# Performance work log

Hardware: AMD Instinct MI355X
Metric: run time of the kernel (lower is better)

The kernel has to match this reference:

```python
import jax, jax.numpy as jnp
import numpy as np
from jax import lax

B, T, N, NIN, NOUT = 16, 32, 512, 32, 16
STEEP_GJ, STEEP_FIRE, STEEP_IN = 10.0, 10.0, 5.0
INPUT_THRESH, LEAKY_SLOPE = 0.01, 0.01
EDGE_P = 0.05


def setup_inputs() -> dict:
    key = jax.random.key(0)
    ks = jax.random.split(key, 7)
    obs_sequence = jax.random.normal(ks[0], (B, T, NIN), dtype=jnp.float32)
    weights = jax.random.uniform(ks[1], (N, N), dtype=jnp.float32) * 5.0
    thresholds = jax.random.uniform(ks[2], (N,), dtype=jnp.float32) * 5.0
    decay = jax.random.uniform(ks[3], (N,), dtype=jnp.float32) * 0.5
    mask_ex = jax.random.bernoulli(ks[4], EDGE_P, (N, N)).astype(jnp.float32)
    mask_in = jax.random.bernoulli(ks[5], EDGE_P, (N, N)).astype(jnp.float32)
    mask_gj = jax.random.bernoulli(ks[6], EDGE_P, (N, N)).astype(jnp.float32)
    input_indices = jnp.arange(NIN, dtype=jnp.int32)
    output_indices = NIN + jnp.arange(NOUT, dtype=jnp.int32)
    return {"obs_sequence": obs_sequence, "weights": weights, "thresholds": thresholds,
            "decay": decay, "mask_ex": mask_ex, "mask_in": mask_in, "mask_gj": mask_gj,
            "input_indices": input_indices, "output_indices": output_indices}


def reference(obs_sequence, weights, thresholds, decay, mask_ex, mask_in, mask_gj,
              input_indices, output_indices):
    # obs_encoder and action_decoder are identity: obs values drive input neurons,
    # action = E-state of output neurons.
    W_pos = jax.nn.softplus(weights)            # [N,N] (dst, src)
    W_chem = W_pos * (mask_ex - mask_in)        # excitatory minus inhibitory
    W_gj = W_pos * mask_gj                      # gap junctions

    def step(carry, obs_t):
        E, O = carry                            # [B,N] each
        O_h = O.at[:, input_indices].set(obs_t)
        E_h = E.at[:, input_indices].set(obs_t)
        # chemical synapse current: [B,N] @ [N,N]^T
        I_chem = O_h @ W_chem.T
        # gap junction current via O(B,N,N) broadcast, as in original
        diff = O_h[:, None, :] - E_h[:, :, None]          # [B, dst, src]
        direction = jnp.tanh(STEEP_GJ * diff)
        I_gj = jnp.einsum('ds,bs,bds->bd', W_gj, O_h, direction)
        curr = jnp.clip(E_h + I_chem + I_gj, -10.0, 10.0)
        z = curr - thresholds
        O_new = jnp.where(z >= 0, z, LEAKY_SLOPE * z)      # leaky_relu
        firing_gate = jax.nn.sigmoid(STEEP_FIRE * z)
        decay_gate = jax.nn.sigmoid(STEEP_IN * (jnp.abs(E_h - curr) - INPUT_THRESH))
        E_nonfired = decay_gate * curr + (1.0 - decay_gate) * (E_h - decay)
        E_new = firing_gate * O_new + (1.0 - firing_gate) * E_nonfired
        O_new = O_new.at[:, input_indices].set(obs_t)
        E_new = E_new.at[:, input_indices].set(obs_t)
        action = E_new[:, output_indices]
        return (E_new, O_new), action

    b, n = obs_sequence.shape[0], weights.shape[0]
    E0 = jnp.zeros((b, n), dtype=obs_sequence.dtype)
    O0 = jnp.zeros((b, n), dtype=obs_sequence.dtype)
    (_, _), actions = lax.scan(step, (E0, O0), jnp.swapaxes(obs_sequence, 0, 1))
    return jnp.swapaxes(actions, 0, 1)                    # [B,T,NOUT]
```

## Files before the change

kernel.cpp:

```cpp
#include <hip/hip_runtime.h>

#define N_NEUR 512
#define B_SZ   16
#define T_STEPS 32
#define NIN    32
#define NOUT   16
#define CAPC   84
#define CAPG   52
#define MC     42
#define MG     26
#define MCP    21
#define MGP    13
#define SLACKC 6
#define SLACKG 6
#define LOG2E  1.4426950408889634f

__device__ __forceinline__ float rcp_fast(float x) {
#if __has_builtin(__builtin_amdgcn_rcpf)
    return __builtin_amdgcn_rcpf(x);
#else
    return 1.0f / x;
#endif
}
__device__ __forceinline__ float exp2_fast(float x) {
#if __has_builtin(__builtin_amdgcn_exp2f)
    return __builtin_amdgcn_exp2f(x);
#else
    return exp2f(x);
#endif
}
__device__ __forceinline__ float pair_swap(float x) {
#if __has_builtin(__builtin_amdgcn_mov_dpp)
    return __int_as_float(__builtin_amdgcn_mov_dpp(__float_as_int(x), 0xB1, 0xF, 0xF, true));
#else
    return __shfl_xor(x, 1);
#endif
}

__global__ __launch_bounds__(64) void prep1_kernel(
    const float* __restrict__ W,
    const float* __restrict__ mex,
    const float* __restrict__ min_,
    const float* __restrict__ mgj,
    int* __restrict__ key_arr, int* __restrict__ ccA, int* __restrict__ cgA,
    int2* __restrict__ tmpC, int2* __restrict__ tmpG)
{
    const int row  = blockIdx.x;
    const int lane = threadIdx.x;
    const unsigned long long below = (1ull << lane) - 1ull;
    int bc = 0, bg = 0;
    for (int c0 = 0; c0 < N_NEUR; c0 += 64) {
        const int col = c0 + lane;
        const int off = row * N_NEUR + col;
        const float w  = W[off];
        const float sp = fmaxf(w, 0.0f) + log1pf(__expf(-fabsf(w)));
        const float dm = mex[off] - min_[off];
        bool a = (dm != 0.0f);
        unsigned long long m = __ballot(a);
        int idx = bc + __popcll(m & below);
        if (a && idx < CAPC)
            tmpC[row * CAPC + idx] = make_int2(col, __float_as_int(sp * dm));
        bc += __popcll(m);

        const float g = mgj[off];
        bool ag = (g != 0.0f);
        m = __ballot(ag);
        idx = bg + __popcll(m & below);
        if (ag && idx < CAPG)
            tmpG[row * CAPG + idx] = make_int2(col, __float_as_int(sp * g));
        bg += __popcll(m);
    }
    if (lane == 0) {
        int cc = min(bc, CAPC), cg = min(bg, CAPG);
        ccA[row] = cc; cgA[row] = cg; key_arr[row] = cc + cg;
    }
}

__global__ __launch_bounds__(512) void rank_kernel(
    int* __restrict__ key_then_rank,
    const int* __restrict__ ccA, const int* __restrict__ cgA,
    int* __restrict__ order, int* __restrict__ mCwA, int* __restrict__ mGwA)
{
    __shared__ int keyS[N_NEUR];
    __shared__ int mxc[16], mxg[16];
    const int d = threadIdx.x;
    keyS[d] = key_then_rank[d];
    if (d < 16) { mxc[d] = 0; mxg[d] = 0; }
    __syncthreads();
    const int kd = keyS[d];
    int r = 0;
    #pragma unroll 8
    for (int j = 0; j < N_NEUR; ++j) {
        int kj = keyS[j];
        r += (kj < kd) || (kj == kd && j < d);
    }
    order[r] = d;
    key_then_rank[d] = r;
    atomicMax(&mxc[r >> 5], ccA[d]);
    atomicMax(&mxg[r >> 5], cgA[d]);
    __syncthreads();
    if (d < 16) {
        int mc = ((mxc[d] + 1) >> 1) + SLACKC;
        mc = (mc + 3) & ~3;
        mCwA[d] = min(mc, MC);
        int mg = ((mxg[d] + 1) >> 1) + SLACKG;
        mg = (mg + 3) & ~3;
        mGwA[d] = min(mg, MG);
    }
}

__global__ __launch_bounds__(64) void prep2_kernel(
    const int* __restrict__ rankA, const int* __restrict__ ccA, const int* __restrict__ cgA,
    const int* __restrict__ mCwA, const int* __restrict__ mGwA,
    const int2* __restrict__ tmpC, const int2* __restrict__ tmpG,
    float* __restrict__ wCt, unsigned* __restrict__ cpCt,
    float* __restrict__ wGt, unsigned* __restrict__ cpGt)
{
    __shared__ int   cS[CAPC];  __shared__ float wS[CAPC];
    __shared__ int   cSg[CAPG]; __shared__ float wSg[CAPG];
    __shared__ int   keyS[MC];
    __shared__ int   scol[MC];  __shared__ float sw[MC];
    __shared__ float wOut[MC];  __shared__ int   oOut[MC];
    const int d    = blockIdx.x;
    const int lane = threadIdx.x;
    const int r    = rankA[d];
    const int wv   = r >> 5;
    const int Lb   = 2 * (r & 31);
    const int cc = ccA[d], cg = cgA[d];
    const int Mc = mCwA[wv], Mg = mGwA[wv];

    for (int k = lane; k < CAPC; k += 64) {
        int2 e = (k < cc) ? tmpC[d * CAPC + k] : make_int2(0, 0);
        cS[k] = e.x; wS[k] = __int_as_float(e.y);
    }
    for (int k = lane; k < CAPG; k += 64) {
        int2 e = (k < cg) ? tmpG[d * CAPG + k] : make_int2(0, 0);
        cSg[k] = e.x; wSg[k] = __int_as_float(e.y);
    }
    __syncthreads();

    #pragma unroll
    for (int task = 0; task < 4; ++task) {
        const int isG  = task >> 1, h = task & 1;
        const int cnt  = isG ? cg : cc;
        const int m    = (cnt + 1 - h) >> 1;
        const int M    = isG ? Mg : Mc;
        const int Mcap = isG ? MG : MC;
        const int MPc  = isG ? MGP : MCP;
        const int myL  = Lb + h;

        int col = 0; float w = 0.0f; int key = 0;
        if (lane < m) {
            col = isG ? cSg[2 * lane + h] : cS[2 * lane + h];
            w   = isG ? wSg[2 * lane + h] : wS[2 * lane + h];
            key = ((col & 31) - myL) & 31;
            keyS[lane] = key;
        }
        __syncthreads();
        if (lane < m) {
            int rk = 0;
            for (int j = 0; j < m; ++j) {
                int kj = keyS[j];
                rk += (kj < key) || (kj == key && j < lane);
            }
            scol[rk] = col; sw[rk] = w;
        }
        if (lane < Mcap) {
            wOut[lane] = 0.0f;
            int bk = (((lane * 32) / M) + myL) & 31;
            oOut[lane] = bk << 2;
        }
        __syncthreads();

        int a = -(1 << 28);
        int colj = 0; float wj = 0.0f;
        if (lane < m) {
            colj = scol[lane]; wj = sw[lane];
            int kj = ((colj & 31) - myL) & 31;
            a = ((kj * M) >> 5) - lane;
        }
        #pragma unroll
        for (int o = 1; o < 64; o <<= 1) {
            int t2 = __shfl_up(a, o);
            if (lane >= o) a = max(a, t2);
        }
        if (lane < m) {
            int slot = min(lane + a, M - m + lane);
            wOut[slot] = wj;
            oOut[slot] = colj << 2;
        }
        __syncthreads();

        float*    wT = isG ? wGt  : wCt;
        unsigned* cT = isG ? cpGt : cpCt;
        if (lane < Mcap)
            wT[(wv * Mcap + lane) * 64 + myL] = wOut[lane];
        if (lane < MPc) {
            unsigned c0 = (unsigned)oOut[2 * lane];
            unsigned c1 = (unsigned)oOut[2 * lane + 1];
            cT[(wv * MPc + lane) * 64 + myL] = c0 | (c1 << 16);
        }
        __syncthreads();
    }
}

#define CHEM_K(k, A) {                                                      \
    unsigned pk = cpC[(k) >> 1];                                            \
    unsigned off = ((k) & 1) ? (pk >> 16) : (pk & 0xffffu);                 \
    A = fmaf(wC[k], *(const float*)((const char*)ObP + off), A); }

#define CHEM_C4(a) { CHEM_K(a, accA) CHEM_K((a)+1, accB) CHEM_K((a)+2, accA) CHEM_K((a)+3, accB) }

#define GJ_K(k, A) {                                                        \
    unsigned pk = cpG[(k) >> 1];                                            \
    unsigned off = ((k) & 1) ? (pk >> 16) : (pk & 0xffffu);                 \
    float Os = *(const float*)((const char*)ObP + off);                     \
    float f = fmaf(20.0f * LOG2E, Os, cE);                                  \
    float tnh = 1.0f - 2.0f * rcp_fast(1.0f + exp2_fast(f));                \
    A = fmaf(wG[k] * Os, tnh, A); }

#define GJ_C4(a) { GJ_K(a, accA) GJ_K((a)+1, accB) GJ_K((a)+2, accA) GJ_K((a)+3, accB) }

__global__ __launch_bounds__(1024, 1) void recur_kernel(
    const float* __restrict__ obs,
    const float* __restrict__ thr,
    const float* __restrict__ dec,
    const int* __restrict__ order,
    const int* __restrict__ mCwA, const int* __restrict__ mGwA,
    const float* __restrict__ wCt, const unsigned* __restrict__ cpCt,
    const float* __restrict__ wGt, const unsigned* __restrict__ cpGt,
    float* __restrict__ out)
{
    __shared__ float Ob[2][N_NEUR];
    __shared__ float Eb[2][N_NEUR];

    const int b    = blockIdx.x;
    const int tid  = threadIdx.x;
    const int h    = tid & 1;
    const int r    = tid >> 1;
    const int wv   = tid >> 6;
    const int lane = tid & 63;

    const int d = order[r];
    const float thr_d = thr[d];
    const float dec_d = dec[d];

    const int mCw = __builtin_amdgcn_readfirstlane(mCwA[wv]);
    const int mGw = __builtin_amdgcn_readfirstlane(mGwA[wv]);

    float wC[MC]; unsigned cpC[MCP];
    float wG[MG]; unsigned cpG[MGP];
    #pragma unroll
    for (int k = 0; k < MC; ++k)  wC[k]  = wCt[(wv * MC + k) * 64 + lane];
    #pragma unroll
    for (int k = 0; k < MCP; ++k) cpC[k] = cpCt[(wv * MCP + k) * 64 + lane];
    #pragma unroll
    for (int k = 0; k < MG; ++k)  wG[k]  = wGt[(wv * MG + k) * 64 + lane];
    #pragma unroll
    for (int k = 0; k < MGP; ++k) cpG[k] = cpGt[(wv * MGP + k) * 64 + lane];

    const bool inj = (h == 0) && (d < NIN);
    const bool wr  = (h == 0) && (d >= NIN) && (d < NIN + NOUT);
    float* outp = out + (size_t)b * T_STEPS * NOUT + (d - NIN);
    const float* obs_b = obs + b * (T_STEPS * NIN);

    if (h == 0) {
        float v = (d < NIN) ? obs_b[d] : 0.0f;
        Ob[0][d] = v;
        Eb[0][d] = v;
    }
    int p = 0;
    __syncthreads();

    for (int t = 0; t < T_STEPS; ++t) {
        float ob_next = (inj && (t + 1 < T_STEPS)) ? obs_b[(t + 1) * NIN + d] : 0.0f;

        const float* ObP = Ob[p];
        const float E_d = Eb[p][d];
        float accA = 0.0f, accB = 0.0f;
        CHEM_C4(0)
        if ( 4 < mCw) CHEM_C4(4)
        if ( 8 < mCw) CHEM_C4(8)
        if (12 < mCw) CHEM_C4(12)
        if (16 < mCw) CHEM_C4(16)
        if (20 < mCw) CHEM_C4(20)
        if (24 < mCw) CHEM_C4(24)
        if (28 < mCw) CHEM_C4(28)
        if (32 < mCw) CHEM_C4(32)
        if (36 < mCw) CHEM_C4(36)
        if (40 < mCw) { CHEM_K(40, accA) CHEM_K(41, accB) }
        const float cE = -20.0f * LOG2E * E_d;
        GJ_C4(0)
        if ( 4 < mGw) GJ_C4(4)
        if ( 8 < mGw) GJ_C4(8)
        if (12 < mGw) GJ_C4(12)
        if (16 < mGw) GJ_C4(16)
        if (20 < mGw) GJ_C4(20)
        if (24 < mGw) { GJ_K(24, accA) GJ_K(25, accB) }

        float acc = accA + accB;
        acc += pair_swap(acc);

        float curr = fminf(fmaxf(E_d + acc, -10.0f), 10.0f);
        float z = curr - thr_d;
        float O_new = (z >= 0.0f) ? z : 0.01f * z;
        float fg = rcp_fast(1.0f + exp2_fast(-10.0f * LOG2E * z));
        float dg = rcp_fast(1.0f + exp2_fast(-5.0f * LOG2E * (fabsf(E_d - curr) - 0.01f)));
        float E_nf  = dg * curr + (1.0f - dg) * (E_d - dec_d);
        float E_new = fg * O_new + (1.0f - fg) * E_nf;

        const int q = p ^ 1;
        if (h == 0) {
            Eb[q][d] = inj ? ob_next : E_new;
            Ob[q][d] = inj ? ob_next : O_new;
            if (wr) outp[t * NOUT] = E_new;
        }
        __syncthreads();
        p = q;
    }
}

extern "C" void kernel_launch(void* const* d_in, const int* in_sizes, int n_in,
                              void* d_out, int out_size, void* d_ws, size_t ws_size,
                              hipStream_t stream)
{
    const float* obs  = (const float*)d_in[0];
    const float* W    = (const float*)d_in[1];
    const float* thr  = (const float*)d_in[2];
    const float* dec  = (const float*)d_in[3];
    const float* mex  = (const float*)d_in[4];
    const float* min_ = (const float*)d_in[5];
    const float* mgj  = (const float*)d_in[6];
    float* out = (float*)d_out;

    char* ws = (char*)d_ws;
    int*   key_arr = (int*)(ws);
    int*   ccA     = (int*)(ws + 2048);
    int*   cgA     = (int*)(ws + 4096);
    int*   order   = (int*)(ws + 6144);
    int2*  tmpC    = (int2*)(ws + 8192);
    int2*  tmpG    = (int2*)(ws + 8192 + 344064);
    float* wCt     = (float*)(ws + 565248);
    unsigned* cpCt = (unsigned*)(ws + 737280);
    float* wGt     = (float*)(ws + 823296);
    unsigned* cpGt = (unsigned*)(ws + 929792);
    int*   mCwA    = (int*)(ws + 983040);
    int*   mGwA    = (int*)(ws + 983104);

    prep1_kernel<<<N_NEUR, 64, 0, stream>>>(W, mex, min_, mgj,
                                            key_arr, ccA, cgA, tmpC, tmpG);
    rank_kernel<<<1, 512, 0, stream>>>(key_arr, ccA, cgA, order, mCwA, mGwA);
    prep2_kernel<<<N_NEUR, 64, 0, stream>>>(key_arr, ccA, cgA, mCwA, mGwA,
                                            tmpC, tmpG, wCt, cpCt, wGt, cpGt);
    recur_kernel<<<B_SZ, 1024, 0, stream>>>(obs, thr, dec,
                                            order, mCwA, mGwA,
                                            wCt, cpCt, wGt, cpGt, out);
}
```

Before: 214.7 us.

## Replicate O buffer at bank-shifted offsets to cut LDS conflicts, keep E in registers

Each step now stores the O state three times in shared memory at staggered offsets (545, 1090). The prep pass assigns each edge slot a copy whose bank matches the slot's target, using a greedy serial scheduler and allowing up to two banks of slip. This is meant to cut LDS bank conflicts in the gather loops. E is now kept in a register per thread instead of a shared buffer, and the chem and gap-junction loops are interleaved. The cost is three shared-memory writes per neuron per step, a single-lane serial loop in prep, and a slightly smaller per-wave slot budget.

```diff
diff --git a/kernel.cpp b/kernel.cpp
--- a/kernel.cpp
+++ b/kernel.cpp
@@ -11,8 +11,9 @@
 #define MG     26
 #define MCP    21
 #define MGP    13
-#define SLACKC 6
-#define SLACKG 6
+#define OB_C1  545
+#define OB_C2  1090
+#define OB_STRIDE 1632
 #define LOG2E  1.4426950408889634f
 
 __device__ __forceinline__ float rcp_fast(float x) {
@@ -100,11 +101,9 @@
     atomicMax(&mxg[r >> 5], cgA[d]);
     __syncthreads();
     if (d < 16) {
-        int mc = ((mxc[d] + 1) >> 1) + SLACKC;
-        mc = (mc + 3) & ~3;
+        int mc = (((mxc[d] + 1) >> 1) + 5) & ~3;
         mCwA[d] = min(mc, MC);
-        int mg = ((mxg[d] + 1) >> 1) + SLACKG;
-        mg = (mg + 3) & ~3;
+        int mg = (((mxg[d] + 1) >> 1) + 5) & ~3;
         mGwA[d] = min(mg, MG);
     }
 }
@@ -120,7 +119,7 @@
     __shared__ int   cSg[CAPG]; __shared__ float wSg[CAPG];
     __shared__ int   keyS[MC];
     __shared__ int   scol[MC];  __shared__ float sw[MC];
-    __shared__ float wOut[MC];  __shared__ int   oOut[MC];
+    __shared__ int   oOut[MC];  __shared__ float wOut[MC];
     const int d    = blockIdx.x;
     const int lane = threadIdx.x;
     const int r    = rankA[d];
@@ -165,29 +164,42 @@
             }
             scol[rk] = col; sw[rk] = w;
         }
-        if (lane < Mcap) {
-            wOut[lane] = 0.0f;
-            int bk = (((lane * 32) / M) + myL) & 31;
-            oOut[lane] = bk << 2;
-        }
-        __syncthreads();
-
-        int a = -(1 << 28);
-        int colj = 0; float wj = 0.0f;
-        if (lane < m) {
-            colj = scol[lane]; wj = sw[lane];
-            int kj = ((colj & 31) - myL) & 31;
-            a = ((kj * M) >> 5) - lane;
-        }
-        #pragma unroll
-        for (int o = 1; o < 64; o <<= 1) {
-            int t2 = __shfl_up(a, o);
-            if (lane >= o) a = max(a, t2);
-        }
-        if (lane < m) {
-            int slot = min(lane + a, M - m + lane);
-            wOut[slot] = wj;
-            oOut[slot] = colj << 2;
+        __syncthreads();
+
+        if (lane == 0) {
+            int j = 0, nOv = 0;
+            for (int k = 0; k < M; ++k) {
+                int v = (k * 32) / M;
+                while (j < m && (((scol[j] & 31) - myL) & 31) + 2 < v) {
+                    keyS[nOv++] = j;
+                    ++j;
+                }
+                int kap = (j < m) ? ((((scol[j] & 31) - myL)) & 31) : 99;
+                if (j < m && kap <= v) {
+                    int rho = v - kap;
+                    int base = (rho == 0) ? 0 : ((rho == 1) ? OB_C1 : OB_C2);
+                    oOut[k] = (scol[j] + base) << 2;
+                    wOut[k] = sw[j];
+                    ++j;
+                } else {
+                    oOut[k] = -1;
+                }
+            }
+            while (j < m) { keyS[nOv++] = j; ++j; }
+            int kf = 0;
+            for (int o = 0; o < nOv; ++o) {
+                while (oOut[kf] >= 0) ++kf;
+                int jj = keyS[o];
+                oOut[kf] = scol[jj] << 2;
+                wOut[kf] = sw[jj];
+            }
+            for (int k = 0; k < M; ++k)
+                if (oOut[k] < 0) {
+                    int dc = (((k * 32) / M) + myL) & 31;
+                    oOut[k] = dc << 2;
+                    wOut[k] = 0.0f;
+                }
+            for (int k = M; k < Mcap; ++k) { oOut[k] = 0; wOut[k] = 0.0f; }
         }
         __syncthreads();
 
@@ -231,8 +243,7 @@
     const float* __restrict__ wGt, const unsigned* __restrict__ cpGt,
     float* __restrict__ out)
 {
-    __shared__ float Ob[2][N_NEUR];
-    __shared__ float Eb[2][N_NEUR];
+    __shared__ float Ob[2][OB_STRIDE];
 
     const int b    = blockIdx.x;
     const int tid  = threadIdx.x;
@@ -259,44 +270,40 @@
     #pragma unroll
     for (int k = 0; k < MGP; ++k) cpG[k] = cpGt[(wv * MGP + k) * 64 + lane];
 
-    const bool inj = (h == 0) && (d < NIN);
-    const bool wr  = (h == 0) && (d >= NIN) && (d < NIN + NOUT);
+    const bool injD = (d < NIN);
+    const bool wr   = (h == 0) && (d >= NIN) && (d < NIN + NOUT);
     float* outp = out + (size_t)b * T_STEPS * NOUT + (d - NIN);
     const float* obs_b = obs + b * (T_STEPS * NIN);
 
-    if (h == 0) {
-        float v = (d < NIN) ? obs_b[d] : 0.0f;
-        Ob[0][d] = v;
-        Eb[0][d] = v;
-    }
+    float E_d = injD ? obs_b[d] : 0.0f;
+    if (h == 0) { Ob[0][d] = E_d; Ob[0][OB_C1 + d] = E_d; Ob[0][OB_C2 + d] = E_d; }
     int p = 0;
     __syncthreads();
 
     for (int t = 0; t < T_STEPS; ++t) {
-        float ob_next = (inj && (t + 1 < T_STEPS)) ? obs_b[(t + 1) * NIN + d] : 0.0f;
+        float ob_next = (injD && (t + 1 < T_STEPS)) ? obs_b[(t + 1) * NIN + d] : 0.0f;
 
         const float* ObP = Ob[p];
-        const float E_d = Eb[p][d];
         float accA = 0.0f, accB = 0.0f;
+        const float cE = -20.0f * LOG2E * E_d;
         CHEM_C4(0)
+        GJ_C4(0)
         if ( 4 < mCw) CHEM_C4(4)
+        if ( 4 < mGw) GJ_C4(4)
         if ( 8 < mCw) CHEM_C4(8)
+        if ( 8 < mGw) GJ_C4(8)
         if (12 < mCw) CHEM_C4(12)
+        if (12 < mGw) GJ_C4(12)
         if (16 < mCw) CHEM_C4(16)
+        if (16 < mGw) GJ_C4(16)
         if (20 < mCw) CHEM_C4(20)
+        if (20 < mGw) GJ_C4(20)
         if (24 < mCw) CHEM_C4(24)
+        if (24 < mGw) { GJ_K(24, accA) GJ_K(25, accB) }
         if (28 < mCw) CHEM_C4(28)
         if (32 < mCw) CHEM_C4(32)
         if (36 < mCw) CHEM_C4(36)
         if (40 < mCw) { CHEM_K(40, accA) CHEM_K(41, accB) }
-        const float cE = -20.0f * LOG2E * E_d;
-        GJ_C4(0)
-        if ( 4 < mGw) GJ_C4(4)
-        if ( 8 < mGw) GJ_C4(8)
-        if (12 < mGw) GJ_C4(12)
-        if (16 < mGw) GJ_C4(16)
-        if (20 < mGw) GJ_C4(20)
-        if (24 < mGw) { GJ_K(24, accA) GJ_K(25, accB) }
 
         float acc = accA + accB;
         acc += pair_swap(acc);
@@ -311,10 +318,11 @@
 
         const int q = p ^ 1;
         if (h == 0) {
-            Eb[q][d] = inj ? ob_next : E_new;
-            Ob[q][d] = inj ? ob_next : O_new;
+            float Ov = injD ? ob_next : O_new;
+            Ob[q][d] = Ov; Ob[q][OB_C1 + d] = Ov; Ob[q][OB_C2 + d] = Ov;
             if (wr) outp[t * NOUT] = E_new;
         }
+        E_d = injD ? ob_next : E_new;
         __syncthreads();
         p = q;
     }
```

Result: slower. 228.7 us (+6.5%).
